# Kernel optimization log

Hardware: AMD Instinct MI355X
Metric: run time of the kernel (lower is better)

Reference implementation:

```python
import jax, jax.numpy as jnp
import numpy as np

B, S, HID = 2, 2048, 1024
H, HKV, D = 16, 16, 64


def _rope_tables(seq_len, dim, base=10000.0):
    inv_freq = 1.0 / (base ** (np.arange(0, dim, 2, dtype=np.float32) / dim))
    t = np.arange(seq_len, dtype=np.float32)
    freqs = np.outer(t, inv_freq)            # [S, D/2]
    emb = np.concatenate([freqs, freqs], axis=-1)  # [S, D]
    return jnp.asarray(np.cos(emb)), jnp.asarray(np.sin(emb))


def setup_inputs() -> dict:
    key = jax.random.key(0)
    k1, k2, k3 = jax.random.split(key, 3)
    hidden_states = jax.random.normal(k1, (B, S, HID), dtype=jnp.float32)
    cos, sin = _rope_tables(S, D)
    w_qkv = jax.random.normal(k2, ((H + 2 * HKV) * D, HID), dtype=jnp.float32) / np.sqrt(HID)
    w_o = jax.random.normal(k3, (HID, H * D), dtype=jnp.float32) / np.sqrt(H * D)
    return {"hidden_states": hidden_states, "cos": cos, "sin": sin, "w_qkv": w_qkv, "w_o": w_o}


def _rotate_half(x):
    mid = x.shape[-1] // 2
    return jnp.concatenate([-x[..., mid:], x[..., :mid]], axis=-1)


def reference(hidden_states, cos, sin, w_qkv, w_o):
    b, s, _ = hidden_states.shape
    qkv = hidden_states @ w_qkv.T                       # [B,S,(H+2HKV)*D]
    qkv = qkv.reshape(b, s, H + 2 * HKV, D).transpose(0, 2, 1, 3)  # [B,heads,S,D]
    q, k, v = qkv[:, :H], qkv[:, H:H + HKV], qkv[:, H + HKV:]
    # RoPE (cos/sin broadcast [S,D] -> [B,H,S,D])
    q = q * cos + _rotate_half(q) * sin
    k = k * cos + _rotate_half(k) * sin
    # causal SDPA
    scale = 1.0 / jnp.sqrt(jnp.asarray(D, dtype=q.dtype))
    scores = jnp.einsum("bhqd,bhkd->bhqk", q, k) * scale
    causal = jnp.tril(jnp.ones((s, s), dtype=bool))
    scores = jnp.where(causal, scores, jnp.finfo(scores.dtype).min)
    attn = jax.nn.softmax(scores, axis=-1)
    out = jnp.einsum("bhqk,bhkd->bhqd", attn, v)        # [B,H,S,D]
    out = out.transpose(0, 2, 1, 3).reshape(b, s, H * D)
    return out @ w_o.T
```

## Files before the change

kernel.cpp:

```cpp
#include <hip/hip_runtime.h>

typedef __bf16 bf16_t;
typedef __bf16 bf16x8 __attribute__((ext_vector_type(8)));
typedef __bf16 bf16x4 __attribute__((ext_vector_type(4)));
typedef float  f32x4  __attribute__((ext_vector_type(4)));
typedef unsigned int u32;
typedef u32 u32x2 __attribute__((ext_vector_type(2)));
typedef u32 u32x4 __attribute__((ext_vector_type(4)));

#define LOG2E 1.44269504088896340736f

__device__ __forceinline__ void gload_lds16(const void* g, void* l) {
  __builtin_amdgcn_global_load_lds(
      (const __attribute__((address_space(1))) void*)g,
      (__attribute__((address_space(3))) void*)l, 16, 0, 0);
}

__device__ __forceinline__ void store_c(float* p, float v)  { *p = v; }
__device__ __forceinline__ void store_c(bf16_t* p, float v) { *p = (bf16_t)v; }

__global__ __launch_bounds__(256) void cast_kernel(const float* __restrict__ in,
                                                   bf16_t* __restrict__ out, int n4) {
  int i = blockIdx.x * 256 + threadIdx.x;
  const int stride = gridDim.x * 256;
  for (; i < n4; i += stride) {
    f32x4 v = *(const f32x4*)(in + (size_t)i * 4);
    bf16x4 o;
#pragma unroll
    for (int j = 0; j < 4; ++j) o[j] = (bf16_t)v[j];
    *(bf16x4*)(out + (size_t)i * 4) = o;
  }
}

template <typename OutT>
__global__ __launch_bounds__(256) void gemm_bt(const bf16_t* __restrict__ A,
                                               const bf16_t* __restrict__ B,
                                               OutT* __restrict__ C,
                                               int M, int N, int K) {
  __shared__ bf16_t As[128 * 32];
  __shared__ bf16_t Bs[128 * 32];
  const int tid  = threadIdx.x;
  const int lane = tid & 63;
  const int wid  = tid >> 6;
  const int wm = wid >> 1, wn = wid & 1;
  const size_t m0 = (size_t)blockIdx.y * 128;
  const size_t n0 = (size_t)blockIdx.x * 128;

  f32x4 acc[4][4] = {};

  for (int k0 = 0; k0 < K; k0 += 32) {
#pragma unroll
    for (int j = 0; j < 2; ++j) {
      const int c = tid + j * 256;
      const int r = c >> 2;
      const int kp = (c & 3) * 8;
      gload_lds16(A + (m0 + r) * K + k0 + kp, As + (size_t)c * 8);
      gload_lds16(B + (n0 + r) * K + k0 + kp, Bs + (size_t)c * 8);
    }
    __syncthreads();

    const int kk = (lane >> 4) * 8;
    const int rs = lane & 15;
    bf16x8 af[4], bfv[4];
#pragma unroll
    for (int t = 0; t < 4; ++t) {
      af[t]  = *(const bf16x8*)(As + (wm * 64 + t * 16 + rs) * 32 + kk);
      bfv[t] = *(const bf16x8*)(Bs + (wn * 64 + t * 16 + rs) * 32 + kk);
    }
#pragma unroll
    for (int mt = 0; mt < 4; ++mt)
#pragma unroll
      for (int nt = 0; nt < 4; ++nt)
        acc[mt][nt] = __builtin_amdgcn_mfma_f32_16x16x32_bf16(af[mt], bfv[nt], acc[mt][nt], 0, 0, 0);
    __syncthreads();
  }

#pragma unroll
  for (int mt = 0; mt < 4; ++mt)
#pragma unroll
    for (int nt = 0; nt < 4; ++nt)
#pragma unroll
      for (int r = 0; r < 4; ++r) {
        size_t row = m0 + wm * 64 + mt * 16 + (lane >> 4) * 4 + r;
        size_t col = n0 + wn * 64 + nt * 16 + (lane & 15);
        store_c(C + row * N + col, acc[mt][nt][r]);
      }
}

__global__ __launch_bounds__(256) void rope_reorg(const bf16_t* __restrict__ qkv,
                                                  const float* __restrict__ cosT,
                                                  const float* __restrict__ sinT,
                                                  bf16_t* __restrict__ Q,
                                                  bf16_t* __restrict__ Kd,
                                                  bf16_t* __restrict__ Vt) {
  __shared__ bf16_t T[64 * 72];
  const int blk  = blockIdx.x;
  const int sblk = blk & 31;
  const int hh   = (blk >> 5) % 48;
  const int b    = blk / (32 * 48);
  const int s0   = sblk * 64;
  const int tid  = threadIdx.x;

  if (hh < 32) {
    const bool isq = hh < 16;
    const int h = isq ? hh : hh - 16;
    bf16_t* dst = (isq ? Q : Kd) + (size_t)(b * 16 + h) * 2048 * 64;
    for (int u = tid; u < 512; u += 256) {
      const int s = u >> 3, oct = u & 7;
      const size_t src = ((size_t)(b * 2048) + s0 + s) * 3072 + hh * 64;
      bf16x8 x = *(const bf16x8*)(qkv + src + oct * 8);
      bf16x8 y = *(const bf16x8*)(qkv + src + ((oct * 8) ^ 32));
      const float* cp = cosT + (size_t)(s0 + s) * 64 + oct * 8;
      const float* sp = sinT + (size_t)(s0 + s) * 64 + oct * 8;
      const float sgn = (oct < 4) ? -1.f : 1.f;
      bf16x8 ov;
#pragma unroll
      for (int j = 0; j < 8; ++j) {
        float xv = (float)x[j], yv = (float)y[j];
        ov[j] = (bf16_t)(xv * cp[j] + sgn * yv * sp[j]);
      }
      *(bf16x8*)(dst + (size_t)(s0 + s) * 64 + oct * 8) = ov;
    }
  } else {
    const int hv = hh - 32;
    for (int u = tid; u < 512; u += 256) {
      const int s = u >> 3, oct = u & 7;
      *(bf16x8*)(&T[s * 72 + oct * 8]) =
          *(const bf16x8*)(qkv + ((size_t)(b * 2048) + s0 + s) * 3072 + hh * 64 + oct * 8);
    }
    __syncthreads();
    bf16_t* dst = Vt + (size_t)(b * 16 + hv) * 64 * 2048;
    for (int u = tid; u < 512; u += 256) {
      const int d = u >> 3, soct = u & 7;
      bf16x8 w;
#pragma unroll
      for (int j = 0; j < 8; ++j) w[j] = T[(soct * 8 + j) * 72 + d];
      *(bf16x8*)(dst + (size_t)d * 2048 + s0 + soct * 8) = w;
    }
  }
}

__global__ __launch_bounds__(256) void attn_kernel(const bf16_t* __restrict__ Q,
                                                   const bf16_t* __restrict__ Kt,
                                                   const bf16_t* __restrict__ Vt,
                                                   bf16_t* __restrict__ O) {
  const int bid  = blockIdx.x;
  const int xcd  = bid & 7;
  const int idx  = bid >> 3;
  const int bh   = xcd * 4 + (idx & 3);
  const int qblk = 31 - (idx >> 2);
  const int b    = bh >> 4;
  const int h    = bh & 15;
  const int tid  = threadIdx.x;
  const int lane = tid & 63;
  const int wid  = tid >> 6;
  const bf16_t* Qb = Q  + (size_t)bh * 2048 * 64;
  const bf16_t* Kb = Kt + (size_t)bh * 2048 * 64;
  const bf16_t* Vb = Vt + (size_t)bh * 64 * 2048;

  const int q0  = qblk * 64 + wid * 16;
  const int l15 = lane & 15;
  const int g   = lane >> 4;
  const int g4  = g * 4;
  const int dd  = g * 8;
  const int qg  = q0 + l15;
  const int qmax = q0 + 15;
  const int ntiles = qblk + 1;
  const float SC = 0.125f * LOG2E;

  bf16x8 qf0 = *(const bf16x8*)(Qb + (size_t)qg * 64 + dd);
  bf16x8 qf1 = *(const bf16x8*)(Qb + (size_t)qg * 64 + 32 + dd);

  f32x4 o[4] = {};
  float m_run = -3.0e38f, l_run = 0.f;

  auto prefK = [&](int tt, bf16x8 (&kf)[4][2]) {
    if (tt >= ntiles) return;
    const int kv0 = tt * 64;
#pragma unroll
    for (int kt = 0; kt < 4; ++kt) {
      const bf16_t* kp = Kb + (size_t)(kv0 + kt * 16 + l15) * 64;
      kf[kt][0] = *(const bf16x8*)(kp + dd);
      kf[kt][1] = *(const bf16x8*)(kp + 32 + dd);
    }
  };
  auto prefV = [&](int tt, bf16x4 (&vl)[2][4], bf16x4 (&vh)[2][4]) {
    if (tt >= ntiles) return;
    const int kv0 = tt * 64;
#pragma unroll
    for (int c = 0; c < 2; ++c)
#pragma unroll
      for (int dt = 0; dt < 4; ++dt) {
        const bf16_t* vp = Vb + (size_t)(dt * 16 + l15) * 2048 + kv0 + 32 * c + g4;
        vl[c][dt] = *(const bf16x4*)(vp);
        vh[c][dt] = *(const bf16x4*)(vp + 16);
      }
  };

  auto join = [](bf16x4 lo, bf16x4 hi2) -> bf16x8 {
    u32x2 a = __builtin_bit_cast(u32x2, lo);
    u32x2 c = __builtin_bit_cast(u32x2, hi2);
    u32x4 w = {a[0], a[1], c[0], c[1]};
    return __builtin_bit_cast(bf16x8, w);
  };

  auto compute = [&](bf16x8 (&kf)[4][2], bf16x4 (&vl)[2][4], bf16x4 (&vh)[2][4],
                     int kv0) {
    f32x4 st[4];
#pragma unroll
    for (int kt = 0; kt < 4; ++kt) {
      f32x4 acc = {};
      acc = __builtin_amdgcn_mfma_f32_16x16x32_bf16(kf[kt][0], qf0, acc, 0, 0, 0);
      acc = __builtin_amdgcn_mfma_f32_16x16x32_bf16(kf[kt][1], qf1, acc, 0, 0, 0);
      st[kt] = acc;
    }

    if (kv0 + 63 > q0) {
#pragma unroll
      for (int kt = 0; kt < 4; ++kt)
#pragma unroll
        for (int r = 0; r < 4; ++r) {
          const int kg = kv0 + kt * 16 + g4 + r;
          st[kt][r] = (kg > qg) ? -1.0e30f : st[kt][r];
        }
    }

    float mb = -3.0e38f;
#pragma unroll
    for (int kt = 0; kt < 4; ++kt) {
      float a = fmaxf(st[kt][0], st[kt][1]);
      float bm = fmaxf(st[kt][2], st[kt][3]);
      mb = fmaxf(mb, fmaxf(a, bm));
    }
    mb = fmaxf(mb, __shfl_xor(mb, 16));
    mb = fmaxf(mb, __shfl_xor(mb, 32));

    const float mn = fmaxf(m_run, mb);
    const float al = __builtin_amdgcn_exp2f((m_run - mn) * SC);
    m_run = mn;
    const float mc = mn * SC;

    float p[4][4];
    float lb = 0.f;
#pragma unroll
    for (int kt = 0; kt < 4; ++kt)
#pragma unroll
      for (int r = 0; r < 4; ++r) {
        p[kt][r] = __builtin_amdgcn_exp2f(__builtin_fmaf(st[kt][r], SC, -mc));
        lb += p[kt][r];
      }
    lb += __shfl_xor(lb, 16);
    lb += __shfl_xor(lb, 32);
    l_run = l_run * al + lb;

#pragma unroll
    for (int dt = 0; dt < 4; ++dt)
#pragma unroll
      for (int r = 0; r < 4; ++r) o[dt][r] *= al;

    bf16x8 pf0, pf1;
#pragma unroll
    for (int j = 0; j < 4; ++j) {
      pf0[j]     = (bf16_t)p[0][j];
      pf0[j + 4] = (bf16_t)p[1][j];
      pf1[j]     = (bf16_t)p[2][j];
      pf1[j + 4] = (bf16_t)p[3][j];
    }

#pragma unroll
    for (int dt = 0; dt < 4; ++dt)
      o[dt] = __builtin_amdgcn_mfma_f32_16x16x32_bf16(join(vl[0][dt], vh[0][dt]), pf0, o[dt], 0, 0, 0);
    if (kv0 + 32 <= qmax) {
#pragma unroll
      for (int dt = 0; dt < 4; ++dt)
        o[dt] = __builtin_amdgcn_mfma_f32_16x16x32_bf16(join(vl[1][dt], vh[1][dt]), pf1, o[dt], 0, 0, 0);
    }
  };

  bf16x8 ka[4][2], kb2[4][2];
  bf16x4 vcl[2][4], vch[2][4];
  prefK(0, ka);
  for (int t = 0; t < ntiles; t += 2) {
    prefK(t + 1, kb2);
    prefV(t, vcl, vch);
    compute(ka, vcl, vch, t * 64);
    prefK(t + 2, ka);
    prefV(t + 1, vcl, vch);
    if (t + 1 < ntiles) compute(kb2, vcl, vch, (t + 1) * 64);
  }

  const float inv = 1.f / l_run;
  bf16_t* Ob = O + ((size_t)(b * 2048) + qg) * 1024 + h * 64;
#pragma unroll
  for (int dt = 0; dt < 4; ++dt) {
    bf16x4 w;
#pragma unroll
    for (int r = 0; r < 4; ++r) w[r] = (bf16_t)(o[dt][r] * inv);
    *(bf16x4*)(Ob + dt * 16 + g4) = w;
  }
}

extern "C" void kernel_launch(void* const* d_in, const int* in_sizes, int n_in,
                              void* d_out, int out_size, void* d_ws, size_t ws_size,
                              hipStream_t stream) {
  const float* hs   = (const float*)d_in[0];
  const float* cosT = (const float*)d_in[1];
  const float* sinT = (const float*)d_in[2];
  const float* wqkv = (const float*)d_in[3];
  const float* wo   = (const float*)d_in[4];
  float* out = (float*)d_out;

  char* ws = (char*)d_ws;
  bf16_t* hs_b   = (bf16_t*)(ws);
  bf16_t* wqkv_b = (bf16_t*)(ws + 8388608);
  bf16_t* wo_b   = (bf16_t*)(ws + 14680064);
  bf16_t* qkv    = (bf16_t*)(ws + 16777216);
  bf16_t* Qb     = (bf16_t*)(ws + 41943040);
  bf16_t* Kb     = (bf16_t*)(ws + 50331648);
  bf16_t* Vtb    = (bf16_t*)(ws + 58720256);
  bf16_t* aout   = (bf16_t*)(ws + 67108864);

  cast_kernel<<<2048, 256, 0, stream>>>(hs,   hs_b,   4194304 / 4);
  cast_kernel<<<1024, 256, 0, stream>>>(wqkv, wqkv_b, 3145728 / 4);
  cast_kernel<<<512,  256, 0, stream>>>(wo,   wo_b,   1048576 / 4);

  gemm_bt<bf16_t><<<dim3(24, 32), 256, 0, stream>>>(hs_b, wqkv_b, qkv, 4096, 3072, 1024);

  rope_reorg<<<3072, 256, 0, stream>>>(qkv, cosT, sinT, Qb, Kb, Vtb);

  attn_kernel<<<1024, 256, 0, stream>>>(Qb, Kb, Vtb, aout);

  gemm_bt<float><<<dim3(8, 32), 256, 0, stream>>>(aout, wo_b, out, 4096, 1024, 1024);
}
```

Baseline: 343.2 us.

## Pair causal query blocks per workgroup and single-buffer K/V prefetch

Each attention workgroup now processes two query blocks, qblk 31-pj and pj, so every block does the same total causal work, and the grid is halved to 512. The double-buffered K tile prefetch is replaced by a single buffer that loads the next tile's K right after the QK MFMAs and the next tile's V after the PV MFMAs. Launch bounds now request 2 blocks per SM to cap register use. The aim is to remove tail imbalance from uneven causal tile counts. The trade-off is less latency hiding for loads and fewer workgroups in flight.

```diff
diff --git a/kernel.cpp b/kernel.cpp
--- a/kernel.cpp
+++ b/kernel.cpp
@@ -140,62 +140,31 @@
   }
 }
 
-__global__ __launch_bounds__(256) void attn_kernel(const bf16_t* __restrict__ Q,
-                                                   const bf16_t* __restrict__ Kt,
-                                                   const bf16_t* __restrict__ Vt,
-                                                   bf16_t* __restrict__ O) {
+__global__ __launch_bounds__(256, 2) void attn_kernel(const bf16_t* __restrict__ Q,
+                                                      const bf16_t* __restrict__ Kt,
+                                                      const bf16_t* __restrict__ Vt,
+                                                      bf16_t* __restrict__ O) {
   const int bid  = blockIdx.x;
   const int xcd  = bid & 7;
   const int idx  = bid >> 3;
   const int bh   = xcd * 4 + (idx & 3);
-  const int qblk = 31 - (idx >> 2);
+  const int pj   = idx >> 2;
   const int b    = bh >> 4;
   const int h    = bh & 15;
   const int tid  = threadIdx.x;
   const int lane = tid & 63;
   const int wid  = tid >> 6;
+  const int l15  = lane & 15;
+  const int g    = lane >> 4;
+  const int g4   = g * 4;
+  const int dd   = g * 8;
   const bf16_t* Qb = Q  + (size_t)bh * 2048 * 64;
   const bf16_t* Kb = Kt + (size_t)bh * 2048 * 64;
   const bf16_t* Vb = Vt + (size_t)bh * 64 * 2048;
-
-  const int q0  = qblk * 64 + wid * 16;
-  const int l15 = lane & 15;
-  const int g   = lane >> 4;
-  const int g4  = g * 4;
-  const int dd  = g * 8;
-  const int qg  = q0 + l15;
-  const int qmax = q0 + 15;
-  const int ntiles = qblk + 1;
   const float SC = 0.125f * LOG2E;
 
-  bf16x8 qf0 = *(const bf16x8*)(Qb + (size_t)qg * 64 + dd);
-  bf16x8 qf1 = *(const bf16x8*)(Qb + (size_t)qg * 64 + 32 + dd);
-
-  f32x4 o[4] = {};
-  float m_run = -3.0e38f, l_run = 0.f;
-
-  auto prefK = [&](int tt, bf16x8 (&kf)[4][2]) {
-    if (tt >= ntiles) return;
-    const int kv0 = tt * 64;
-#pragma unroll
-    for (int kt = 0; kt < 4; ++kt) {
-      const bf16_t* kp = Kb + (size_t)(kv0 + kt * 16 + l15) * 64;
-      kf[kt][0] = *(const bf16x8*)(kp + dd);
-      kf[kt][1] = *(const bf16x8*)(kp + 32 + dd);
-    }
-  };
-  auto prefV = [&](int tt, bf16x4 (&vl)[2][4], bf16x4 (&vh)[2][4]) {
-    if (tt >= ntiles) return;
-    const int kv0 = tt * 64;
-#pragma unroll
-    for (int c = 0; c < 2; ++c)
-#pragma unroll
-      for (int dt = 0; dt < 4; ++dt) {
-        const bf16_t* vp = Vb + (size_t)(dt * 16 + l15) * 2048 + kv0 + 32 * c + g4;
-        vl[c][dt] = *(const bf16x4*)(vp);
-        vh[c][dt] = *(const bf16x4*)(vp + 16);
-      }
-  };
+  bf16x8 kf[4][2];
+  bf16x4 vl[2][4], vh[2][4];
 
   auto join = [](bf16x4 lo, bf16x4 hi2) -> bf16x8 {
     u32x2 a = __builtin_bit_cast(u32x2, lo);
@@ -204,99 +173,138 @@
     return __builtin_bit_cast(bf16x8, w);
   };
 
-  auto compute = [&](bf16x8 (&kf)[4][2], bf16x4 (&vl)[2][4], bf16x4 (&vh)[2][4],
-                     int kv0) {
-    f32x4 st[4];
+  for (int phase = 0; phase < 2; ++phase) {
+    const int qblk = (phase == 0) ? (31 - pj) : pj;
+    const int q0   = qblk * 64 + wid * 16;
+    const int qg   = q0 + l15;
+    const int ntiles = qblk + 1;
+
+    bf16x8 qf0 = *(const bf16x8*)(Qb + (size_t)qg * 64 + dd);
+    bf16x8 qf1 = *(const bf16x8*)(Qb + (size_t)qg * 64 + 32 + dd);
+
+    f32x4 o[4] = {};
+    float m_run = -3.0e38f, l_run = 0.f;
+
 #pragma unroll
     for (int kt = 0; kt < 4; ++kt) {
-      f32x4 acc = {};
-      acc = __builtin_amdgcn_mfma_f32_16x16x32_bf16(kf[kt][0], qf0, acc, 0, 0, 0);
-      acc = __builtin_amdgcn_mfma_f32_16x16x32_bf16(kf[kt][1], qf1, acc, 0, 0, 0);
-      st[kt] = acc;
-    }
-
-    if (kv0 + 63 > q0) {
-#pragma unroll
-      for (int kt = 0; kt < 4; ++kt)
+      const bf16_t* kp = Kb + (size_t)(kt * 16 + l15) * 64;
+      kf[kt][0] = *(const bf16x8*)(kp + dd);
+      kf[kt][1] = *(const bf16x8*)(kp + 32 + dd);
+    }
+#pragma unroll
+    for (int c = 0; c < 2; ++c)
+#pragma unroll
+      for (int dt = 0; dt < 4; ++dt) {
+        const bf16_t* vp = Vb + (size_t)(dt * 16 + l15) * 2048 + 32 * c + g4;
+        vl[c][dt] = *(const bf16x4*)(vp);
+        vh[c][dt] = *(const bf16x4*)(vp + 16);
+      }
+
+    for (int t = 0; t < ntiles; ++t) {
+      const int kv0 = t * 64;
+
+      f32x4 st[4];
+#pragma unroll
+      for (int kt = 0; kt < 4; ++kt) {
+        f32x4 acc = {};
+        acc = __builtin_amdgcn_mfma_f32_16x16x32_bf16(kf[kt][0], qf0, acc, 0, 0, 0);
+        acc = __builtin_amdgcn_mfma_f32_16x16x32_bf16(kf[kt][1], qf1, acc, 0, 0, 0);
+        st[kt] = acc;
+      }
+
+      if (t + 1 < ntiles) {
+        const int kn = kv0 + 64;
+#pragma unroll
+        for (int kt = 0; kt < 4; ++kt) {
+          const bf16_t* kp = Kb + (size_t)(kn + kt * 16 + l15) * 64;
+          kf[kt][0] = *(const bf16x8*)(kp + dd);
+          kf[kt][1] = *(const bf16x8*)(kp + 32 + dd);
+        }
+      }
+
+      if (kv0 + 63 > q0) {
+#pragma unroll
+        for (int kt = 0; kt < 4; ++kt)
+#pragma unroll
+          for (int r = 0; r < 4; ++r) {
+            const int kg = kv0 + kt * 16 + g4 + r;
+            st[kt][r] = (kg > qg) ? -1.0e30f : st[kt][r];
+          }
+      }
+
+      float mb = -3.0e38f;
+#pragma unroll
+      for (int kt = 0; kt < 4; ++kt) {
+        float a = fmaxf(st[kt][0], st[kt][1]);
+        float bm = fmaxf(st[kt][2], st[kt][3]);
+        mb = fmaxf(mb, fmaxf(a, bm));
+      }
+      mb = fmaxf(mb, __shfl_xor(mb, 16));
+      mb = fmaxf(mb, __shfl_xor(mb, 32));
+
+      const float mn = fmaxf(m_run, mb);
+      const float al = __builtin_amdgcn_exp2f((m_run - mn) * SC);
+      m_run = mn;
+      const float mc = mn * SC;
+
+      float lb = 0.f;
+      bf16x8 pf0, pf1;
+#pragma unroll
+      for (int kt = 0; kt < 4; ++kt) {
+        float pv[4];
 #pragma unroll
         for (int r = 0; r < 4; ++r) {
-          const int kg = kv0 + kt * 16 + g4 + r;
-          st[kt][r] = (kg > qg) ? -1.0e30f : st[kt][r];
+          pv[r] = __builtin_amdgcn_exp2f(__builtin_fmaf(st[kt][r], SC, -mc));
+          lb += pv[r];
         }
-    }
-
-    float mb = -3.0e38f;
-#pragma unroll
-    for (int kt = 0; kt < 4; ++kt) {
-      float a = fmaxf(st[kt][0], st[kt][1]);
-      float bm = fmaxf(st[kt][2], st[kt][3]);
-      mb = fmaxf(mb, fmaxf(a, bm));
-    }
-    mb = fmaxf(mb, __shfl_xor(mb, 16));
-    mb = fmaxf(mb, __shfl_xor(mb, 32));
-
-    const float mn = fmaxf(m_run, mb);
-    const float al = __builtin_amdgcn_exp2f((m_run - mn) * SC);
-    m_run = mn;
-    const float mc = mn * SC;
-
-    float p[4][4];
-    float lb = 0.f;
-#pragma unroll
-    for (int kt = 0; kt < 4; ++kt)
-#pragma unroll
-      for (int r = 0; r < 4; ++r) {
-        p[kt][r] = __builtin_amdgcn_exp2f(__builtin_fmaf(st[kt][r], SC, -mc));
-        lb += p[kt][r];
-      }
-    lb += __shfl_xor(lb, 16);
-    lb += __shfl_xor(lb, 32);
-    l_run = l_run * al + lb;
-
-#pragma unroll
-    for (int dt = 0; dt < 4; ++dt)
-#pragma unroll
-      for (int r = 0; r < 4; ++r) o[dt][r] *= al;
-
-    bf16x8 pf0, pf1;
-#pragma unroll
-    for (int j = 0; j < 4; ++j) {
-      pf0[j]     = (bf16_t)p[0][j];
-      pf0[j + 4] = (bf16_t)p[1][j];
-      pf1[j]     = (bf16_t)p[2][j];
-      pf1[j + 4] = (bf16_t)p[3][j];
-    }
-
-#pragma unroll
-    for (int dt = 0; dt < 4; ++dt)
-      o[dt] = __builtin_amdgcn_mfma_f32_16x16x32_bf16(join(vl[0][dt], vh[0][dt]), pf0, o[dt], 0, 0, 0);
-    if (kv0 + 32 <= qmax) {
+#pragma unroll
+        for (int r = 0; r < 4; ++r) {
+          if (kt == 0) pf0[r]     = (bf16_t)pv[r];
+          if (kt == 1) pf0[r + 4] = (bf16_t)pv[r];
+          if (kt == 2) pf1[r]     = (bf16_t)pv[r];
+          if (kt == 3) pf1[r + 4] = (bf16_t)pv[r];
+        }
+      }
+      lb += __shfl_xor(lb, 16);
+      lb += __shfl_xor(lb, 32);
+      l_run = l_run * al + lb;
+
 #pragma unroll
       for (int dt = 0; dt < 4; ++dt)
-        o[dt] = __builtin_amdgcn_mfma_f32_16x16x32_bf16(join(vl[1][dt], vh[1][dt]), pf1, o[dt], 0, 0, 0);
-    }
-  };
-
-  bf16x8 ka[4][2], kb2[4][2];
-  bf16x4 vcl[2][4], vch[2][4];
-  prefK(0, ka);
-  for (int t = 0; t < ntiles; t += 2) {
-    prefK(t + 1, kb2);
-    prefV(t, vcl, vch);
-    compute(ka, vcl, vch, t * 64);
-    prefK(t + 2, ka);
-    prefV(t + 1, vcl, vch);
-    if (t + 1 < ntiles) compute(kb2, vcl, vch, (t + 1) * 64);
-  }
-
-  const float inv = 1.f / l_run;
-  bf16_t* Ob = O + ((size_t)(b * 2048) + qg) * 1024 + h * 64;
-#pragma unroll
-  for (int dt = 0; dt < 4; ++dt) {
-    bf16x4 w;
-#pragma unroll
-    for (int r = 0; r < 4; ++r) w[r] = (bf16_t)(o[dt][r] * inv);
-    *(bf16x4*)(Ob + dt * 16 + g4) = w;
+#pragma unroll
+        for (int r = 0; r < 4; ++r) o[dt][r] *= al;
+
+#pragma unroll
+      for (int dt = 0; dt < 4; ++dt)
+        o[dt] = __builtin_amdgcn_mfma_f32_16x16x32_bf16(join(vl[0][dt], vh[0][dt]), pf0, o[dt], 0, 0, 0);
+      if (kv0 + 32 <= q0 + 15) {
+#pragma unroll
+        for (int dt = 0; dt < 4; ++dt)
+          o[dt] = __builtin_amdgcn_mfma_f32_16x16x32_bf16(join(vl[1][dt], vh[1][dt]), pf1, o[dt], 0, 0, 0);
+      }
+
+      if (t + 1 < ntiles) {
+        const int kn = kv0 + 64;
+#pragma unroll
+        for (int c = 0; c < 2; ++c)
+#pragma unroll
+          for (int dt = 0; dt < 4; ++dt) {
+            const bf16_t* vp = Vb + (size_t)(dt * 16 + l15) * 2048 + kn + 32 * c + g4;
+            vl[c][dt] = *(const bf16x4*)(vp);
+            vh[c][dt] = *(const bf16x4*)(vp + 16);
+          }
+      }
+    }
+
+    const float inv = 1.f / l_run;
+    bf16_t* Ob = O + ((size_t)(b * 2048) + qg) * 1024 + h * 64;
+#pragma unroll
+    for (int dt = 0; dt < 4; ++dt) {
+      bf16x4 w;
+#pragma unroll
+      for (int r = 0; r < 4; ++r) w[r] = (bf16_t)(o[dt][r] * inv);
+      *(bf16x4*)(Ob + dt * 16 + g4) = w;
+    }
   }
 }
 
@@ -328,7 +336,7 @@
 
   rope_reorg<<<3072, 256, 0, stream>>>(qkv, cosT, sinT, Qb, Kb, Vtb);
 
-  attn_kernel<<<1024, 256, 0, stream>>>(Qb, Kb, Vtb, aout);
+  attn_kernel<<<512, 256, 0, stream>>>(Qb, Kb, Vtb, aout);
 
   gemm_bt<float><<<dim3(8, 32), 256, 0, stream>>>(aout, wo_b, out, 4096, 1024, 1024);
 }
```

New measurement: 334.5 us. 2.5% less time.
